# Performance work log

Measured on AMD Instinct MI355X. Metric: run time of the kernel, lower is better.

## Reference

```python
import jax, jax.numpy as jnp
import numpy as np

N = 100_000          # nodes
E = 3_200_000        # edges (avg degree 32)
EMB = 16             # item embedding dim
IN = EMB + 1         # concat(embed, scalar feature)
HID = 32             # GAT hidden size
NEMB = 1000          # embedding vocab
SLOPE = 0.2          # GATConv leaky_relu negative slope


def setup_inputs() -> dict:
    key = jax.random.key(0)
    ks = jax.random.split(key, 24)
    g = lambda k, shape, fan: jax.random.normal(k, shape, dtype=jnp.float32) * (1.0 / np.sqrt(fan))
    inp = {
        "x_ids": jax.random.randint(ks[0], (N,), 0, NEMB, dtype=jnp.int32),
        "x_feat": jax.random.normal(ks[1], (N, 1), dtype=jnp.float32),
        "src": jax.random.randint(ks[2], (E,), 0, N, dtype=jnp.int32),
        "dst": jax.random.randint(ks[3], (E,), 0, N, dtype=jnp.int32),
        "edge_attr": jax.random.normal(ks[4], (E, 1), dtype=jnp.float32),
        # embedding table
        "emb": g(ks[5], (NEMB, EMB), EMB),
        # GATConv 1 (in=17, out=32, heads=1, edge_dim=1)
        "W1": g(ks[6], (IN, HID), IN),
        "a_s1": g(ks[7], (HID,), HID),
        "a_d1": g(ks[8], (HID,), HID),
        "We1": g(ks[9], (1, HID), 1),
        "a_e1": g(ks[10], (HID,), HID),
        "b1": jnp.zeros((HID,), jnp.float32),
        # GATConv 2 (in=32, out=32)
        "W2": g(ks[11], (HID, HID), HID),
        "a_s2": g(ks[12], (HID,), HID),
        "a_d2": g(ks[13], (HID,), HID),
        "We2": g(ks[14], (1, HID), 1),
        "a_e2": g(ks[15], (HID,), HID),
        "b2": jnp.zeros((HID,), jnp.float32),
        # final linear (32 -> 1)
        "lin_w": g(ks[16], (HID, 1), HID),
        "lin_b": jnp.zeros((1,), jnp.float32),
    }
    return inp


def _gat_conv(x, src, dst, eattr, W, a_s, a_d, We, a_e, b):
    """PyG GATConv (heads=1, concat=True) with edge features, self-loops already added."""
    h = x @ W                                   # [N, HID]
    alpha_src = h @ a_s                         # [N]
    alpha_dst = h @ a_d                         # [N]
    alpha_edge = (eattr @ We) @ a_e             # [E']
    alpha = jax.nn.leaky_relu(alpha_src[src] + alpha_dst[dst] + alpha_edge, SLOPE)
    # segment softmax over incoming edges of each dst node
    m = jax.ops.segment_max(alpha, dst, num_segments=N)
    ex = jnp.exp(alpha - m[dst])
    denom = jax.ops.segment_sum(ex, dst, num_segments=N)
    coef = ex / (denom[dst] + 1e-16)
    out = jax.ops.segment_sum(coef[:, None] * h[src], dst, num_segments=N)
    return out + b


def reference(x_ids, x_feat, src, dst, edge_attr, emb,
              W1, a_s1, a_d1, We1, a_e1, b1,
              W2, a_s2, a_d2, We2, a_e2, b2,
              lin_w, lin_b):
    # embedding lookup + concat scalar feature -> [N, 17]
    x = jnp.concatenate([emb[x_ids], x_feat], axis=1)

    # add self-loops once; self-loop edge_attr = mean of incoming edge attrs (fill_value='mean')
    loop = jnp.arange(N, dtype=src.dtype)
    deg = jax.ops.segment_sum(jnp.ones((E,), x.dtype), dst, num_segments=N)
    loop_attr = jax.ops.segment_sum(edge_attr, dst, num_segments=N) / jnp.maximum(deg, 1.0)[:, None]
    src2 = jnp.concatenate([src, loop])
    dst2 = jnp.concatenate([dst, loop])
    ea2 = jnp.concatenate([edge_attr, loop_attr], axis=0)

    x = _gat_conv(x, src2, dst2, ea2, W1, a_s1, a_d1, We1, a_e1, b1)
    x = jax.nn.relu(x)  # dropout is identity in eval mode
    x = _gat_conv(x, src2, dst2, ea2, W2, a_s2, a_d2, We2, a_e2, b2)
    return x @ lin_w + lin_b  # [N, 1]
```

## Files before the change

### kernel.cpp

```cpp
#include <hip/hip_runtime.h>

#define NN 100000
#define EE 3200000
#define SLOPE 0.2f

#define BKN 128
constexpr int NBK = (NN + BKN - 1) / BKN;
#define CAP 4544
constexpr int EP = EE + NN;
#define EPB 4096
constexpr int NBB = (EE + EPB - 1) / EPB;
constexpr int NBT = (NN + 255) / 256;

__global__ void k_bucket(const int* __restrict__ src, const int* __restrict__ dst,
                         const float* __restrict__ ea, int* __restrict__ cnt,
                         int2* __restrict__ stage) {
    __shared__ int hst[NBK];
    __shared__ int scl[NBK];
    __shared__ int gdel[NBK];
    __shared__ int aux[256];
    __shared__ int2 rec[EPB];
    __shared__ int addr[EPB];
    int t = threadIdx.x;
    int base = blockIdx.x * EPB;
    int nedge = min(EPB, EE - base);
    for (int i = t; i < NBK; i += 256) hst[i] = 0;
    __syncthreads();
    int ds[16], ss[16]; float es[16];
#pragma unroll
    for (int j = 0; j < 16; j++) {
        int e = base + j * 256 + t;
        bool v = e < EE;
        ds[j] = v ? dst[e] : -1;
        ss[j] = v ? src[e] : 0;
        es[j] = v ? ea[e] : 0.f;
        if (v) atomicAdd(&hst[ds[j] >> 7], 1);
    }
    __syncthreads();
    int i0 = t * 4;
    int v0 = (i0 + 0 < NBK) ? hst[i0 + 0] : 0;
    int v1 = (i0 + 1 < NBK) ? hst[i0 + 1] : 0;
    int v2 = (i0 + 2 < NBK) ? hst[i0 + 2] : 0;
    int v3 = (i0 + 3 < NBK) ? hst[i0 + 3] : 0;
    int tsum = v0 + v1 + v2 + v3;
    aux[t] = tsum;
    __syncthreads();
    for (int off = 1; off < 256; off <<= 1) {
        int x = (t >= off) ? aux[t - off] : 0;
        __syncthreads();
        aux[t] += x;
        __syncthreads();
    }
    int ex = aux[t] - tsum;
    if (i0 + 0 < NBK) scl[i0 + 0] = ex;
    if (i0 + 1 < NBK) scl[i0 + 1] = ex + v0;
    if (i0 + 2 < NBK) scl[i0 + 2] = ex + v0 + v1;
    if (i0 + 3 < NBK) scl[i0 + 3] = ex + v0 + v1 + v2;
    __syncthreads();
    for (int i = t; i < NBK; i += 256) {
        int hh = hst[i];
        int g = hh ? atomicAdd(&cnt[i], hh) : 0;
        gdel[i] = (g + i * CAP) - scl[i];
    }
    __syncthreads();
#pragma unroll
    for (int j = 0; j < 16; j++) {
        if (ds[j] >= 0) {
            int bk = ds[j] >> 7;
            int pos = atomicAdd(&scl[bk], 1);
            int gpos = pos + gdel[bk];
            rec[pos] = make_int2(ss[j] | ((ds[j] & 127) << 17), __float_as_int(es[j]));
            addr[pos] = (gpos - bk * CAP < CAP) ? gpos : -1;
        }
    }
    __syncthreads();
    for (int i = t; i < nedge; i += 256) {
        int a = addr[i];
        if (a >= 0) stage[a] = rec[i];
    }
}

__global__ void k_scanc(const int* __restrict__ cnt, int* __restrict__ fbase,
                        const float* __restrict__ We1, const float* __restrict__ ae1,
                        const float* __restrict__ We2, const float* __restrict__ ae2,
                        float* __restrict__ cbuf) {
    __shared__ int a[1024];
    int t = threadIdx.x;
    if (blockIdx.x == 1) {
        if (t < 64) {
            int comp = t & 31;
            float p = (t < 32) ? We1[comp] * ae1[comp] : We2[comp] * ae2[comp];
#pragma unroll
            for (int off = 16; off >= 1; off >>= 1) p += __shfl_xor(p, off);
            if (comp == 0) cbuf[t >> 5] = p;
        }
        return;
    }
    int v = 0;
    if (t < NBK) v = min(cnt[t], CAP) + min(BKN, NN - t * BKN);
    a[t] = v;
    __syncthreads();
    for (int off = 1; off < 1024; off <<= 1) {
        int x = (t >= off) ? a[t - off] : 0;
        __syncthreads();
        a[t] += x;
        __syncthreads();
    }
    if (t < NBK) fbase[t] = a[t] - v;
}

__global__ void k_build(const int* __restrict__ cnt, const int* __restrict__ fbase,
                        const int2* __restrict__ stage, int2* __restrict__ csr,
                        int* __restrict__ offs) {
    __shared__ int ldeg[BKN];
    __shared__ float esum[BKN];
    __shared__ int sc[BKN];
    __shared__ int lcur[BKN];
    int b = blockIdx.x, t = threadIdx.x;
    int nbase = b * BKN;
    int npb = min(BKN, NN - nbase);
    int c = min(cnt[b], CAP);
    const int2* ep = stage + (size_t)b * CAP;
    if (t < BKN) { ldeg[t] = 0; esum[t] = 0.f; }
    __syncthreads();
    for (int i = t; i < c; i += 1024) {
        int2 e = ep[i];
        int n = (e.x >> 17) & 127;
        atomicAdd(&ldeg[n], 1);
        atomicAdd(&esum[n], __int_as_float(e.y));
    }
    __syncthreads();
    int v = (t < npb) ? ldeg[t] + 1 : 0;
    if (t < BKN) sc[t] = v;
    __syncthreads();
    for (int off = 1; off < BKN; off <<= 1) {
        int x = (t >= off && t < BKN) ? sc[t - off] : 0;
        __syncthreads();
        if (t < BKN) sc[t] += x;
        __syncthreads();
    }
    if (t < npb) {
        int start = fbase[b] + sc[t] - v;
        offs[nbase + t] = start;
        lcur[t] = start;
    }
    __syncthreads();
    for (int i = t; i < c; i += 1024) {
        int2 e = ep[i];
        int n = (e.x >> 17) & 127;
        int pos = atomicAdd(&lcur[n], 1);
        csr[pos] = make_int2(e.x & 0x1FFFF, e.y);
    }
    __syncthreads();
    if (t < npb) {
        float mean = esum[t] / fmaxf((float)ldeg[t], 1.0f);
        csr[lcur[t]] = make_int2(nbase + t, __float_as_int(mean));
    }
    if (b == 0 && t == 0) offs[NN] = EP;
}


__global__ void k_h1(const int* __restrict__ ids, const float* __restrict__ feat,
                     const float* __restrict__ emb, const float* __restrict__ W,
                     const float* __restrict__ avs, const float* __restrict__ avd,
                     float* __restrict__ h, float* __restrict__ as_, float* __restrict__ ad_) {
    int n = blockIdx.x * 256 + threadIdx.x;
    if (n >= NN) return;
    float hv[32];
#pragma unroll
    for (int j = 0; j < 32; j++) hv[j] = 0.f;
    int id = ids[n];
    const float4* e4 = (const float4*)(emb + (size_t)id * 16);
#pragma unroll
    for (int k4 = 0; k4 < 4; k4++) {
        float4 xv = e4[k4];
        const float* wr = W + k4 * 4 * 32;
#pragma unroll
        for (int j = 0; j < 32; j++)
            hv[j] += xv.x * wr[j] + xv.y * wr[32 + j] + xv.z * wr[64 + j] + xv.w * wr[96 + j];
    }
    float f = feat[n];
#pragma unroll
    for (int j = 0; j < 32; j++) hv[j] += f * W[16 * 32 + j];
    float s = 0.f, d = 0.f;
#pragma unroll
    for (int j = 0; j < 32; j++) { s += hv[j] * avs[j]; d += hv[j] * avd[j]; }
    as_[n] = s;
    ad_[n] = d;
    float4* h4 = (float4*)(h + (size_t)n * 32);
#pragma unroll
    for (int q = 0; q < 8; q++)
        h4[q] = make_float4(hv[4 * q], hv[4 * q + 1], hv[4 * q + 2], hv[4 * q + 3]);
}

__global__ void k_h2(const float* __restrict__ x, const float* __restrict__ W,
                     const float* __restrict__ avs, const float* __restrict__ avd,
                     float* __restrict__ h, float* __restrict__ as_, float* __restrict__ ad_) {
    int n = blockIdx.x * 256 + threadIdx.x;
    if (n >= NN) return;
    float hv[32];
#pragma unroll
    for (int j = 0; j < 32; j++) hv[j] = 0.f;
    const float4* x4 = (const float4*)(x + (size_t)n * 32);
#pragma unroll
    for (int k4 = 0; k4 < 8; k4++) {
        float4 xv = x4[k4];
        const float* wr = W + k4 * 4 * 32;
#pragma unroll
        for (int j = 0; j < 32; j++)
            hv[j] += xv.x * wr[j] + xv.y * wr[32 + j] + xv.z * wr[64 + j] + xv.w * wr[96 + j];
    }
    float s = 0.f, d = 0.f;
#pragma unroll
    for (int j = 0; j < 32; j++) { s += hv[j] * avs[j]; d += hv[j] * avd[j]; }
    as_[n] = s;
    ad_[n] = d;
    float4* h4 = (float4*)(h + (size_t)n * 32);
#pragma unroll
    for (int q = 0; q < 8; q++)
        h4[q] = make_float4(hv[4 * q], hv[4 * q + 1], hv[4 * q + 2], hv[4 * q + 3]);
}

template <bool FINAL>
__global__ void k_gat(const int* __restrict__ offs, const int2* __restrict__ csr,
                      const float* __restrict__ h, const float* __restrict__ as_,
                      const float* __restrict__ ad_, const float* __restrict__ cbuf,
                      int cidx, const float* __restrict__ bias,
                      const float* __restrict__ lw, const float* __restrict__ lb,
                      float* __restrict__ out) {
    __shared__ int2 xb[4][64];
    int wid = threadIdx.x >> 6;
    int node = blockIdx.x * 4 + wid;
    int lane = threadIdx.x & 63;
    int comp = threadIdx.x & 31;
    int slot = (threadIdx.x >> 5) & 1;
    int base = offs[node];
    int cnt = offs[node + 1] - base;
    float c = cbuf[cidx];
    float adn = ad_[node];
    float acc0 = 0.f, acc1 = 0.f, acc2 = 0.f, acc3 = 0.f, exs = 0.f;
    for (int cb = 0; cb < cnt; cb += 64) {
        int idx = cb + lane;
        bool val = idx < cnt;
        int2 e = csr[base + (val ? idx : 0)];
        int s = e.x;
        float a = as_[s] + adn + c * __int_as_float(e.y);
        a = (a >= 0.f) ? a : SLOPE * a;
        float ex = val ? __expf(a) : 0.f;
        exs += ex;
        xb[wid][lane] = make_int2(s << 5, __float_as_int(ex));
        int m = min(cnt - cb, 64);
        for (int j = 0; j < m; j += 8) {
            int2 p0 = xb[wid][j + slot];
            int2 p1 = xb[wid][j + 2 + slot];
            int2 p2 = xb[wid][j + 4 + slot];
            int2 p3 = xb[wid][j + 6 + slot];
            acc0 += __int_as_float(p0.y) * h[p0.x + comp];
            acc1 += __int_as_float(p1.y) * h[p1.x + comp];
            acc2 += __int_as_float(p2.y) * h[p2.x + comp];
            acc3 += __int_as_float(p3.y) * h[p3.x + comp];
        }
    }
    float acc = (acc0 + acc1) + (acc2 + acc3);
    acc += __shfl_xor(acc, 32);
#pragma unroll
    for (int off = 1; off < 64; off <<= 1) exs += __shfl_xor(exs, off);
    float o = acc / (exs + 1e-16f) + bias[comp];
    if (!FINAL) {
        o = fmaxf(o, 0.f);
        if (lane < 32) out[(size_t)node * 32 + comp] = o;
    } else {
        float y = o * lw[comp];
#pragma unroll
        for (int off = 16; off >= 1; off >>= 1) y += __shfl_xor(y, off);
        if (lane == 0) out[node] = y + lb[0];
    }
}


extern "C" void kernel_launch(void* const* d_in, const int* in_sizes, int n_in,
                              void* d_out, int out_size, void* d_ws, size_t ws_size,
                              hipStream_t stream) {
    const int* x_ids = (const int*)d_in[0];
    const float* x_feat = (const float*)d_in[1];
    const int* src = (const int*)d_in[2];
    const int* dst = (const int*)d_in[3];
    const float* eattr = (const float*)d_in[4];
    const float* emb = (const float*)d_in[5];
    const float* W1 = (const float*)d_in[6];
    const float* a_s1 = (const float*)d_in[7];
    const float* a_d1 = (const float*)d_in[8];
    const float* We1 = (const float*)d_in[9];
    const float* a_e1 = (const float*)d_in[10];
    const float* b1 = (const float*)d_in[11];
    const float* W2 = (const float*)d_in[12];
    const float* a_s2 = (const float*)d_in[13];
    const float* a_d2 = (const float*)d_in[14];
    const float* We2 = (const float*)d_in[15];
    const float* a_e2 = (const float*)d_in[16];
    const float* b2 = (const float*)d_in[17];
    const float* lin_w = (const float*)d_in[18];
    const float* lin_b = (const float*)d_in[19];

    char* p = (char*)d_ws;
    auto alloc = [&](size_t bytes) {
        void* r = (void*)p;
        p += (bytes + 255) & ~(size_t)255;
        return r;
    };
    int* cnt = (int*)alloc(NBK * 4);
    int* fbase = (int*)alloc(NBK * 4);
    float* cbuf = (float*)alloc(2 * 4);
    int* offs = (int*)alloc((NN + 1) * 4);
    float* asb1 = (float*)alloc(NN * 4);
    float* adb1 = (float*)alloc(NN * 4);
    float* asb2 = (float*)alloc(NN * 4);
    float* adb2 = (float*)alloc(NN * 4);
    float* h1 = (float*)alloc((size_t)NN * 32 * 4);
    int2* csr = (int2*)alloc((size_t)EP * 8);
    char* regionA = (char*)alloc((size_t)NBK * CAP * 8);
    int2* stage = (int2*)regionA;
    float* x2 = (float*)regionA;
    float* h2 = (float*)(regionA + (size_t)NN * 32 * 4);
    (void)ws_size; (void)in_sizes; (void)n_in; (void)out_size;

    hipMemsetAsync(cnt, 0, NBK * 4, stream);

    const int NW = (NN + 3) / 4;

    k_bucket<<<NBB, 256, 0, stream>>>(src, dst, eattr, cnt, stage);
    k_h1<<<NBT, 256, 0, stream>>>(x_ids, x_feat, emb, W1, a_s1, a_d1, h1, asb1, adb1);
    k_scanc<<<2, 1024, 0, stream>>>(cnt, fbase, We1, a_e1, We2, a_e2, cbuf);
    k_build<<<NBK, 1024, 0, stream>>>(cnt, fbase, stage, csr, offs);
    k_gat<false><<<NW, 256, 0, stream>>>(offs, csr, h1, asb1, adb1, cbuf, 0, b1,
                                         nullptr, nullptr, x2);
    k_h2<<<NBT, 256, 0, stream>>>(x2, W2, a_s2, a_d2, h2, asb2, adb2);
    k_gat<true><<<NW, 256, 0, stream>>>(offs, csr, h2, asb2, adb2, cbuf, 1, b2,
                                        lin_w, lin_b, (float*)d_out);
}
```

Before: 342.7 us.

## Fuse bucketing with layer-1 projection, drop global scan, vectorize GAT gathers

The edge bucketing kernel and the layer-1 node projection are merged into one launch, with block ranges split by role. The global prefix-scan kernel is removed: the CSR now uses fixed per-bucket slots of CAP+BKN entries, and each node stores an (offset, count) pair. The edge-attention constant is computed inside the GAT kernel instead of a separate kernel. The GAT aggregation reads h as float2 with 16 lanes per edge and four edges per step, halving gather instructions. The cost is a padded CSR with gaps between buckets and a redundant per-warp dot product.

```diff
diff --git a/kernel.cpp b/kernel.cpp
--- a/kernel.cpp
+++ b/kernel.cpp
@@ -7,14 +7,19 @@
 #define BKN 128
 constexpr int NBK = (NN + BKN - 1) / BKN;
 #define CAP 4544
-constexpr int EP = EE + NN;
+#define CSLOT (CAP + BKN)
 #define EPB 4096
 constexpr int NBB = (EE + EPB - 1) / EPB;
 constexpr int NBT = (NN + 255) / 256;
 
-__global__ void k_bucket(const int* __restrict__ src, const int* __restrict__ dst,
-                         const float* __restrict__ ea, int* __restrict__ cnt,
-                         int2* __restrict__ stage) {
+__global__ void k_fat(const int* __restrict__ src, const int* __restrict__ dst,
+                      const float* __restrict__ ea, int* __restrict__ cnt,
+                      int2* __restrict__ stage,
+                      const int* __restrict__ ids, const float* __restrict__ feat,
+                      const float* __restrict__ emb, const float* __restrict__ W,
+                      const float* __restrict__ avs, const float* __restrict__ avd,
+                      float* __restrict__ h, float* __restrict__ as_,
+                      float* __restrict__ ad_) {
     __shared__ int hst[NBK];
     __shared__ int scl[NBK];
     __shared__ int gdel[NBK];
@@ -22,96 +27,96 @@
     __shared__ int2 rec[EPB];
     __shared__ int addr[EPB];
     int t = threadIdx.x;
-    int base = blockIdx.x * EPB;
-    int nedge = min(EPB, EE - base);
-    for (int i = t; i < NBK; i += 256) hst[i] = 0;
-    __syncthreads();
-    int ds[16], ss[16]; float es[16];
-#pragma unroll
-    for (int j = 0; j < 16; j++) {
-        int e = base + j * 256 + t;
-        bool v = e < EE;
-        ds[j] = v ? dst[e] : -1;
-        ss[j] = v ? src[e] : 0;
-        es[j] = v ? ea[e] : 0.f;
-        if (v) atomicAdd(&hst[ds[j] >> 7], 1);
-    }
-    __syncthreads();
-    int i0 = t * 4;
-    int v0 = (i0 + 0 < NBK) ? hst[i0 + 0] : 0;
-    int v1 = (i0 + 1 < NBK) ? hst[i0 + 1] : 0;
-    int v2 = (i0 + 2 < NBK) ? hst[i0 + 2] : 0;
-    int v3 = (i0 + 3 < NBK) ? hst[i0 + 3] : 0;
-    int tsum = v0 + v1 + v2 + v3;
-    aux[t] = tsum;
-    __syncthreads();
-    for (int off = 1; off < 256; off <<= 1) {
-        int x = (t >= off) ? aux[t - off] : 0;
-        __syncthreads();
-        aux[t] += x;
-        __syncthreads();
-    }
-    int ex = aux[t] - tsum;
-    if (i0 + 0 < NBK) scl[i0 + 0] = ex;
-    if (i0 + 1 < NBK) scl[i0 + 1] = ex + v0;
-    if (i0 + 2 < NBK) scl[i0 + 2] = ex + v0 + v1;
-    if (i0 + 3 < NBK) scl[i0 + 3] = ex + v0 + v1 + v2;
-    __syncthreads();
-    for (int i = t; i < NBK; i += 256) {
-        int hh = hst[i];
-        int g = hh ? atomicAdd(&cnt[i], hh) : 0;
-        gdel[i] = (g + i * CAP) - scl[i];
-    }
-    __syncthreads();
-#pragma unroll
-    for (int j = 0; j < 16; j++) {
-        if (ds[j] >= 0) {
-            int bk = ds[j] >> 7;
-            int pos = atomicAdd(&scl[bk], 1);
-            int gpos = pos + gdel[bk];
-            rec[pos] = make_int2(ss[j] | ((ds[j] & 127) << 17), __float_as_int(es[j]));
-            addr[pos] = (gpos - bk * CAP < CAP) ? gpos : -1;
-        }
-    }
-    __syncthreads();
-    for (int i = t; i < nedge; i += 256) {
-        int a = addr[i];
-        if (a >= 0) stage[a] = rec[i];
-    }
-}
-
-__global__ void k_scanc(const int* __restrict__ cnt, int* __restrict__ fbase,
-                        const float* __restrict__ We1, const float* __restrict__ ae1,
-                        const float* __restrict__ We2, const float* __restrict__ ae2,
-                        float* __restrict__ cbuf) {
-    __shared__ int a[1024];
-    int t = threadIdx.x;
-    if (blockIdx.x == 1) {
-        if (t < 64) {
-            int comp = t & 31;
-            float p = (t < 32) ? We1[comp] * ae1[comp] : We2[comp] * ae2[comp];
-#pragma unroll
-            for (int off = 16; off >= 1; off >>= 1) p += __shfl_xor(p, off);
-            if (comp == 0) cbuf[t >> 5] = p;
-        }
-        return;
-    }
-    int v = 0;
-    if (t < NBK) v = min(cnt[t], CAP) + min(BKN, NN - t * BKN);
-    a[t] = v;
-    __syncthreads();
-    for (int off = 1; off < 1024; off <<= 1) {
-        int x = (t >= off) ? a[t - off] : 0;
-        __syncthreads();
-        a[t] += x;
-        __syncthreads();
-    }
-    if (t < NBK) fbase[t] = a[t] - v;
-}
-
-__global__ void k_build(const int* __restrict__ cnt, const int* __restrict__ fbase,
-                        const int2* __restrict__ stage, int2* __restrict__ csr,
-                        int* __restrict__ offs) {
+    if (blockIdx.x < NBB) {
+        int base = blockIdx.x * EPB;
+        int nedge = min(EPB, EE - base);
+        for (int i = t; i < NBK; i += 256) hst[i] = 0;
+        __syncthreads();
+        int ds[16], ss[16]; float es[16];
+#pragma unroll
+        for (int j = 0; j < 16; j++) {
+            int e = base + j * 256 + t;
+            bool v = e < EE;
+            ds[j] = v ? dst[e] : -1;
+            ss[j] = v ? src[e] : 0;
+            es[j] = v ? ea[e] : 0.f;
+            if (v) atomicAdd(&hst[ds[j] >> 7], 1);
+        }
+        __syncthreads();
+        int i0 = t * 4;
+        int v0 = (i0 + 0 < NBK) ? hst[i0 + 0] : 0;
+        int v1 = (i0 + 1 < NBK) ? hst[i0 + 1] : 0;
+        int v2 = (i0 + 2 < NBK) ? hst[i0 + 2] : 0;
+        int v3 = (i0 + 3 < NBK) ? hst[i0 + 3] : 0;
+        int tsum = v0 + v1 + v2 + v3;
+        aux[t] = tsum;
+        __syncthreads();
+        for (int off = 1; off < 256; off <<= 1) {
+            int x = (t >= off) ? aux[t - off] : 0;
+            __syncthreads();
+            aux[t] += x;
+            __syncthreads();
+        }
+        int ex = aux[t] - tsum;
+        if (i0 + 0 < NBK) scl[i0 + 0] = ex;
+        if (i0 + 1 < NBK) scl[i0 + 1] = ex + v0;
+        if (i0 + 2 < NBK) scl[i0 + 2] = ex + v0 + v1;
+        if (i0 + 3 < NBK) scl[i0 + 3] = ex + v0 + v1 + v2;
+        __syncthreads();
+        for (int i = t; i < NBK; i += 256) {
+            int hh = hst[i];
+            int g = hh ? atomicAdd(&cnt[i], hh) : 0;
+            gdel[i] = (g + i * CAP) - scl[i];
+        }
+        __syncthreads();
+#pragma unroll
+        for (int j = 0; j < 16; j++) {
+            if (ds[j] >= 0) {
+                int bk = ds[j] >> 7;
+                int pos = atomicAdd(&scl[bk], 1);
+                int gpos = pos + gdel[bk];
+                rec[pos] = make_int2(ss[j] | ((ds[j] & 127) << 17), __float_as_int(es[j]));
+                addr[pos] = (gpos - bk * CAP < CAP) ? gpos : -1;
+            }
+        }
+        __syncthreads();
+        for (int i = t; i < nedge; i += 256) {
+            int a = addr[i];
+            if (a >= 0) stage[a] = rec[i];
+        }
+    } else {
+        int n = (blockIdx.x - NBB) * 256 + t;
+        if (n >= NN) return;
+        float hv[32];
+#pragma unroll
+        for (int j = 0; j < 32; j++) hv[j] = 0.f;
+        int id = ids[n];
+        const float4* e4 = (const float4*)(emb + (size_t)id * 16);
+#pragma unroll
+        for (int k4 = 0; k4 < 4; k4++) {
+            float4 xv = e4[k4];
+            const float* wr = W + k4 * 4 * 32;
+#pragma unroll
+            for (int j = 0; j < 32; j++)
+                hv[j] += xv.x * wr[j] + xv.y * wr[32 + j] + xv.z * wr[64 + j] + xv.w * wr[96 + j];
+        }
+        float f = feat[n];
+#pragma unroll
+        for (int j = 0; j < 32; j++) hv[j] += f * W[16 * 32 + j];
+        float s = 0.f, d = 0.f;
+#pragma unroll
+        for (int j = 0; j < 32; j++) { s += hv[j] * avs[j]; d += hv[j] * avd[j]; }
+        as_[n] = s;
+        ad_[n] = d;
+        float4* h4 = (float4*)(h + (size_t)n * 32);
+#pragma unroll
+        for (int q = 0; q < 8; q++)
+            h4[q] = make_float4(hv[4 * q], hv[4 * q + 1], hv[4 * q + 2], hv[4 * q + 3]);
+    }
+}
+
+__global__ void k_build(const int* __restrict__ cnt, const int2* __restrict__ stage,
+                        int2* __restrict__ csr, int2* __restrict__ offs2) {
     __shared__ int ldeg[BKN];
     __shared__ float esum[BKN];
     __shared__ int sc[BKN];
@@ -121,6 +126,7 @@
     int npb = min(BKN, NN - nbase);
     int c = min(cnt[b], CAP);
     const int2* ep = stage + (size_t)b * CAP;
+    int cbase = b * CSLOT;
     if (t < BKN) { ldeg[t] = 0; esum[t] = 0.f; }
     __syncthreads();
     for (int i = t; i < c; i += 1024) {
@@ -140,8 +146,8 @@
         __syncthreads();
     }
     if (t < npb) {
-        int start = fbase[b] + sc[t] - v;
-        offs[nbase + t] = start;
+        int start = cbase + sc[t] - v;
+        offs2[nbase + t] = make_int2(start, v);
         lcur[t] = start;
     }
     __syncthreads();
@@ -156,41 +162,6 @@
         float mean = esum[t] / fmaxf((float)ldeg[t], 1.0f);
         csr[lcur[t]] = make_int2(nbase + t, __float_as_int(mean));
     }
-    if (b == 0 && t == 0) offs[NN] = EP;
-}
-
-
-__global__ void k_h1(const int* __restrict__ ids, const float* __restrict__ feat,
-                     const float* __restrict__ emb, const float* __restrict__ W,
-                     const float* __restrict__ avs, const float* __restrict__ avd,
-                     float* __restrict__ h, float* __restrict__ as_, float* __restrict__ ad_) {
-    int n = blockIdx.x * 256 + threadIdx.x;
-    if (n >= NN) return;
-    float hv[32];
-#pragma unroll
-    for (int j = 0; j < 32; j++) hv[j] = 0.f;
-    int id = ids[n];
-    const float4* e4 = (const float4*)(emb + (size_t)id * 16);
-#pragma unroll
-    for (int k4 = 0; k4 < 4; k4++) {
-        float4 xv = e4[k4];
-        const float* wr = W + k4 * 4 * 32;
-#pragma unroll
-        for (int j = 0; j < 32; j++)
-            hv[j] += xv.x * wr[j] + xv.y * wr[32 + j] + xv.z * wr[64 + j] + xv.w * wr[96 + j];
-    }
-    float f = feat[n];
-#pragma unroll
-    for (int j = 0; j < 32; j++) hv[j] += f * W[16 * 32 + j];
-    float s = 0.f, d = 0.f;
-#pragma unroll
-    for (int j = 0; j < 32; j++) { s += hv[j] * avs[j]; d += hv[j] * avd[j]; }
-    as_[n] = s;
-    ad_[n] = d;
-    float4* h4 = (float4*)(h + (size_t)n * 32);
-#pragma unroll
-    for (int q = 0; q < 8; q++)
-        h4[q] = make_float4(hv[4 * q], hv[4 * q + 1], hv[4 * q + 2], hv[4 * q + 3]);
 }
 
 __global__ void k_h2(const float* __restrict__ x, const float* __restrict__ W,
@@ -222,57 +193,74 @@
 }
 
 template <bool FINAL>
-__global__ void k_gat(const int* __restrict__ offs, const int2* __restrict__ csr,
+__global__ void k_gat(const int2* __restrict__ offs2, const int2* __restrict__ csr,
                       const float* __restrict__ h, const float* __restrict__ as_,
-                      const float* __restrict__ ad_, const float* __restrict__ cbuf,
-                      int cidx, const float* __restrict__ bias,
+                      const float* __restrict__ ad_,
+                      const float* __restrict__ We, const float* __restrict__ ae,
+                      const float* __restrict__ bias,
                       const float* __restrict__ lw, const float* __restrict__ lb,
                       float* __restrict__ out) {
     __shared__ int2 xb[4][64];
     int wid = threadIdx.x >> 6;
     int node = blockIdx.x * 4 + wid;
     int lane = threadIdx.x & 63;
-    int comp = threadIdx.x & 31;
-    int slot = (threadIdx.x >> 5) & 1;
-    int base = offs[node];
-    int cnt = offs[node + 1] - base;
-    float c = cbuf[cidx];
+    int comp = lane & 31;
+    int cp = (lane & 15) * 2;
+    int slot4 = lane >> 4;
+    float c = We[comp] * ae[comp];
+#pragma unroll
+    for (int off = 1; off < 32; off <<= 1) c += __shfl_xor(c, off);
+    int2 oo = offs2[node];
+    int base = oo.x;
+    int cnt = oo.y;
     float adn = ad_[node];
-    float acc0 = 0.f, acc1 = 0.f, acc2 = 0.f, acc3 = 0.f, exs = 0.f;
+    float2 acc0 = {0.f, 0.f}, acc1 = {0.f, 0.f}, acc2 = {0.f, 0.f}, acc3 = {0.f, 0.f};
+    float exs = 0.f;
     for (int cb = 0; cb < cnt; cb += 64) {
         int idx = cb + lane;
         bool val = idx < cnt;
         int2 e = csr[base + (val ? idx : 0)];
-        int s = e.x;
-        float a = as_[s] + adn + c * __int_as_float(e.y);
+        float a = as_[e.x] + adn + c * __int_as_float(e.y);
         a = (a >= 0.f) ? a : SLOPE * a;
         float ex = val ? __expf(a) : 0.f;
         exs += ex;
-        xb[wid][lane] = make_int2(s << 5, __float_as_int(ex));
+        xb[wid][lane] = make_int2(e.x << 5, __float_as_int(ex));
         int m = min(cnt - cb, 64);
-        for (int j = 0; j < m; j += 8) {
-            int2 p0 = xb[wid][j + slot];
-            int2 p1 = xb[wid][j + 2 + slot];
-            int2 p2 = xb[wid][j + 4 + slot];
-            int2 p3 = xb[wid][j + 6 + slot];
-            acc0 += __int_as_float(p0.y) * h[p0.x + comp];
-            acc1 += __int_as_float(p1.y) * h[p1.x + comp];
-            acc2 += __int_as_float(p2.y) * h[p2.x + comp];
-            acc3 += __int_as_float(p3.y) * h[p3.x + comp];
-        }
-    }
-    float acc = (acc0 + acc1) + (acc2 + acc3);
-    acc += __shfl_xor(acc, 32);
+        for (int j = 0; j < m; j += 16) {
+            int2 p0 = xb[wid][j + slot4];
+            int2 p1 = xb[wid][j + 4 + slot4];
+            int2 p2 = xb[wid][j + 8 + slot4];
+            int2 p3 = xb[wid][j + 12 + slot4];
+            float2 h0 = *(const float2*)(h + p0.x + cp);
+            float2 h1 = *(const float2*)(h + p1.x + cp);
+            float2 h2 = *(const float2*)(h + p2.x + cp);
+            float2 h3 = *(const float2*)(h + p3.x + cp);
+            float w0 = __int_as_float(p0.y), w1 = __int_as_float(p1.y);
+            float w2 = __int_as_float(p2.y), w3 = __int_as_float(p3.y);
+            acc0.x += w0 * h0.x; acc0.y += w0 * h0.y;
+            acc1.x += w1 * h1.x; acc1.y += w1 * h1.y;
+            acc2.x += w2 * h2.x; acc2.y += w2 * h2.y;
+            acc3.x += w3 * h3.x; acc3.y += w3 * h3.y;
+        }
+    }
+    float2 acc;
+    acc.x = (acc0.x + acc1.x) + (acc2.x + acc3.x);
+    acc.y = (acc0.y + acc1.y) + (acc2.y + acc3.y);
+    acc.x += __shfl_xor(acc.x, 16); acc.y += __shfl_xor(acc.y, 16);
+    acc.x += __shfl_xor(acc.x, 32); acc.y += __shfl_xor(acc.y, 32);
 #pragma unroll
     for (int off = 1; off < 64; off <<= 1) exs += __shfl_xor(exs, off);
-    float o = acc / (exs + 1e-16f) + bias[comp];
+    float inv = 1.0f / (exs + 1e-16f);
+    float ox = acc.x * inv + bias[cp];
+    float oy = acc.y * inv + bias[cp + 1];
     if (!FINAL) {
-        o = fmaxf(o, 0.f);
-        if (lane < 32) out[(size_t)node * 32 + comp] = o;
+        ox = fmaxf(ox, 0.f);
+        oy = fmaxf(oy, 0.f);
+        if (lane < 16) *(float2*)(out + (size_t)node * 32 + cp) = make_float2(ox, oy);
     } else {
-        float y = o * lw[comp];
-#pragma unroll
-        for (int off = 16; off >= 1; off >>= 1) y += __shfl_xor(y, off);
+        float y = ox * lw[cp] + oy * lw[cp + 1];
+#pragma unroll
+        for (int off = 1; off < 16; off <<= 1) y += __shfl_xor(y, off);
         if (lane == 0) out[node] = y + lb[0];
     }
 }
@@ -309,15 +297,13 @@
         return r;
     };
     int* cnt = (int*)alloc(NBK * 4);
-    int* fbase = (int*)alloc(NBK * 4);
-    float* cbuf = (float*)alloc(2 * 4);
-    int* offs = (int*)alloc((NN + 1) * 4);
+    int2* offs2 = (int2*)alloc((size_t)NN * 8);
     float* asb1 = (float*)alloc(NN * 4);
     float* adb1 = (float*)alloc(NN * 4);
     float* asb2 = (float*)alloc(NN * 4);
     float* adb2 = (float*)alloc(NN * 4);
     float* h1 = (float*)alloc((size_t)NN * 32 * 4);
-    int2* csr = (int2*)alloc((size_t)EP * 8);
+    int2* csr = (int2*)alloc((size_t)NBK * CSLOT * 8);
     char* regionA = (char*)alloc((size_t)NBK * CAP * 8);
     int2* stage = (int2*)regionA;
     float* x2 = (float*)regionA;
@@ -328,13 +314,13 @@
 
     const int NW = (NN + 3) / 4;
 
-    k_bucket<<<NBB, 256, 0, stream>>>(src, dst, eattr, cnt, stage);
-    k_h1<<<NBT, 256, 0, stream>>>(x_ids, x_feat, emb, W1, a_s1, a_d1, h1, asb1, adb1);
-    k_scanc<<<2, 1024, 0, stream>>>(cnt, fbase, We1, a_e1, We2, a_e2, cbuf);
-    k_build<<<NBK, 1024, 0, stream>>>(cnt, fbase, stage, csr, offs);
-    k_gat<false><<<NW, 256, 0, stream>>>(offs, csr, h1, asb1, adb1, cbuf, 0, b1,
-                                         nullptr, nullptr, x2);
+    k_fat<<<NBB + NBT, 256, 0, stream>>>(src, dst, eattr, cnt, stage,
+                                         x_ids, x_feat, emb, W1, a_s1, a_d1,
+                                         h1, asb1, adb1);
+    k_build<<<NBK, 1024, 0, stream>>>(cnt, stage, csr, offs2);
+    k_gat<false><<<NW, 256, 0, stream>>>(offs2, csr, h1, asb1, adb1,
+                                         We1, a_e1, b1, nullptr, nullptr, x2);
     k_h2<<<NBT, 256, 0, stream>>>(x2, W2, a_s2, a_d2, h2, asb2, adb2);
-    k_gat<true><<<NW, 256, 0, stream>>>(offs, csr, h2, asb2, adb2, cbuf, 1, b2,
-                                        lin_w, lin_b, (float*)d_out);
-}
+    k_gat<true><<<NW, 256, 0, stream>>>(offs2, csr, h2, asb2, adb2,
+                                        We2, a_e2, b2, lin_w, lin_b, (float*)d_out);
+}
```

Result: faster. 328.3 us (-4.2%).
